# Kernel optimization log

Hardware: AMD Instinct MI355X
Metric: run time of the kernel (lower is better)

## Reference

```python
import jax, jax.numpy as jnp
import numpy as np
from jax import lax

CODEBOOK_DIM = 32
SCALE_SCHEDULE = [1, 2, 4, 8, 16, 32, 64, 128, 256, 512, 1024, 2048, 4096, 8192]
INV_TEMP = 100.0
COMMIT_W = 0.2
ENTROPY_W = 0.1
EPS_NORM = 1e-12
EPS_LOG = 1e-8


def setup_inputs() -> dict:
    key = jax.random.key(0)
    B, T, C = 32, 8192, CODEBOOK_DIM
    f_BTC = jax.random.normal(key, (B, T, C), dtype=jnp.float32)
    return {"f_BTC": f_BTC}


def _area_down(x, pt):
    # torch F.interpolate mode='area' on divisible sizes == average pooling
    B, T, C = x.shape
    if pt == T:
        return x
    return x.reshape(B, pt, T // pt, C).mean(axis=2)


def _linear_up(x, out_size):
    # torch F.interpolate mode='linear', align_corners=False
    B, in_size, C = x.shape
    if out_size == in_size:
        return x
    scale = in_size / out_size
    pos = (jnp.arange(out_size, dtype=jnp.float32) + 0.5) * scale - 0.5
    pos = jnp.clip(pos, 0.0, in_size - 1)
    lo = jnp.floor(pos).astype(jnp.int32)
    hi = jnp.minimum(lo + 1, in_size - 1)
    w = (pos - lo.astype(jnp.float32))[None, :, None]
    return x[:, lo] * (1.0 - w) + x[:, hi] * w


def _bsq_level(z):
    # normalize
    norm = jnp.sqrt(jnp.sum(z * z, axis=-1, keepdims=True))
    z = z / jnp.maximum(norm, EPS_NORM)
    q_scale = 1.0 / (CODEBOOK_DIM ** 0.5)
    zhat = jnp.where(z > 0, q_scale, -q_scale).astype(z.dtype)
    quant = z + lax.stop_gradient(zhat - z)  # STE
    # soft entropy loss
    p = jax.nn.sigmoid(-4.0 * z / (CODEBOOK_DIM ** 0.5) * INV_TEMP)
    ent = lambda c: -(c * jnp.log(c + EPS_LOG))
    per_sample = (ent(p) + ent(1.0 - p)).sum(axis=-1).mean()
    avg_p = p.mean(axis=(0, 1))  # [C]
    cb_ent = (ent(avg_p) + ent(1.0 - avg_p)).sum()
    entropy_penalty = (per_sample - cb_ent) / INV_TEMP
    commit = jnp.mean(((lax.stop_gradient(quant) - z) ** 2).sum(axis=-1))
    aux = entropy_penalty * ENTROPY_W + commit * COMMIT_W
    bits = (quant > 0).astype(jnp.int32)
    return quant, bits, aux


def reference(f_BTC):
    B, T, C = f_BTC.shape
    quantized_out = jnp.zeros_like(f_BTC)
    residual = f_BTC
    all_losses, all_bits = [], []
    for pt in SCALE_SCHEDULE:
        r = _area_down(residual, pt)
        quant, bits, loss = _bsq_level(r)
        q_up = _linear_up(quant, T)
        residual = residual - lax.stop_gradient(q_up)
        quantized_out = quantized_out + q_up
        all_bits.append(bits)
        all_losses.append(loss)
    return quantized_out, jnp.concatenate(all_bits, axis=1), jnp.stack(all_losses, axis=-1)
```

## Files before the change

kernel.cpp:

```cpp
#include <hip/hip_runtime.h>

#define B_DIM 32
#define T_DIM 8192
#define C_DIM 32
#define N_ELEM (B_DIM * T_DIM * C_DIM)
#define SUM_PT 16383
#define BITS_ELEM (B_DIM * SUM_PT * C_DIM)
#define NLEVEL 14
#define PARTW 2048
#define QSCALE 0.17677669529663687f
#define ALPHA  70.710678118654755f

#define OWN 128
#define HALO 16
#define MAXL (OWN + 2 * HALO)

__device__ __forceinline__ float entf(float x) { return -(x * __logf(x + 1e-8f)); }
__device__ __forceinline__ float qval(float bit) { return bit * (2.0f * QSCALE) - QSCALE; }

__device__ __forceinline__ float interp_pk(const unsigned int* __restrict__ pkbase,
                                           int ptj, float tpos, int c) {
    const float a = (float)ptj * (1.0f / (float)T_DIM);
    float pos = (tpos + 0.5f) * a - 0.5f;
    pos = fminf(fmaxf(pos, 0.0f), (float)(ptj - 1));
    const int lo = (int)pos;
    const int hi = min(lo + 1, ptj - 1);
    const float w = pos - (float)lo;
    const float b0 = (float)((pkbase[lo] >> c) & 1u);
    const float b1 = (float)((pkbase[hi] >> c) & 1u);
    return ((b0 * (1.0f - w) + b1 * w) * 2.0f - 1.0f) * QSCALE;
}

__device__ __forceinline__ float corr_mid_local(const unsigned int* __restrict__ bl,
                                                int ptk, int row, int c, int p0, int pN) {
    const float a = (float)ptk * (1.0f / (float)T_DIM);
    float pos = (float)(2 * row + 1) * a - 0.5f;
    pos = fminf(fmaxf(pos, 0.0f), (float)(ptk - 1));
    const int lo = (int)pos;
    const int hi = min(lo + 1, ptk - 1);
    const float w = pos - (float)lo;
    const int lol = min(max(lo - p0, 0), pN - 1);
    const int hil = min(max(hi - p0, 0), pN - 1);
    const float b0 = (float)((bl[lol] >> c) & 1u);
    const float b1 = (float)((bl[hil] >> c) & 1u);
    return ((b0 * (1.0f - w) + b1 * w) * 2.0f - 1.0f) * QSCALE;
}

__device__ float pooled_up_sum64(const float* base, int ptj, int m) {
    const int W = 64;
    const float a = (float)ptj * (1.0f / (float)T_DIM);
    const float p0 = ((float)(m * W) + 0.5f) * a - 0.5f;
    const float pmax = (float)(ptj - 1);
    float sum = 0.0f;
    int iL = 0;
    if (p0 < 0.0f) { iL = (int)ceilf(-p0 / a); if (iL > W) iL = W; }
    int iH = W - 1;
    if (p0 + (float)(W - 1) * a > pmax) {
        iH = (int)floorf((pmax - p0) / a);
        if (iH > W - 1) iH = W - 1;
        if (iH < -1) iH = -1;
    }
    if (iL > 0) sum += (float)iL * qval(base[0]);
    if (iH < W - 1) sum += (float)(W - 1 - iH) * qval(base[(size_t)(ptj - 1) * C_DIM]);
    if (iH >= iL) {
        const float pL = p0 + (float)iL * a;
        int l0 = (int)pL;
        if (l0 > ptj - 1) l0 = ptj - 1;
        const int is = (int)ceilf(((float)(l0 + 1) - p0) / a);
        const int endA = min(is - 1, iH);
        if (endA >= iL) {
            const int nA = endA - iL + 1;
            const float sI = 0.5f * (float)(iL + endA) * (float)nA;
            const float SA = (float)nA * (p0 - (float)l0) + a * sI;
            const float q0 = qval(base[(size_t)l0 * C_DIM]);
            const float q1 = qval(base[(size_t)min(l0 + 1, ptj - 1) * C_DIM]);
            sum += (float)nA * q0 + SA * (q1 - q0);
        }
        const int begB = max(is, iL);
        if (begB <= iH) {
            const int nB = iH - begB + 1;
            const float sI = 0.5f * (float)(begB + iH) * (float)nB;
            const float SB = (float)nB * (p0 - (float)(l0 + 1)) + a * sI;
            const float q1 = qval(base[(size_t)min(l0 + 1, ptj - 1) * C_DIM]);
            const float q2 = qval(base[(size_t)min(l0 + 2, ptj - 1) * C_DIM]);
            sum += (float)nB * q1 + SB * (q2 - q1);
        }
    }
    return sum;
}

template <int NT>
__device__ __forceinline__ void write_partials(float eAcc, float cAcc, float pAcc,
                                               float* partial, int level, int col) {
    __shared__ float sP[NT];
    __shared__ float sEC[NT / 16];
    __syncthreads();
    const int grp = threadIdx.x >> 5, c = threadIdx.x & 31;
    float eg = eAcc, cg = cAcc;
#pragma unroll
    for (int m = 16; m >= 1; m >>= 1) { eg += __shfl_xor(eg, m, 32); cg += __shfl_xor(cg, m, 32); }
    if (c == 0) { sEC[grp * 2] = eg; sEC[grp * 2 + 1] = cg; }
    sP[threadIdx.x] = pAcc;
    __syncthreads();
    float* base = partial + (size_t)level * 34 * PARTW;
    if (threadIdx.x < 32) {
        float ps = 0.f;
#pragma unroll
        for (int r = 0; r < NT / 32; ++r) ps += sP[threadIdx.x + r * 32];
        base[(size_t)(2 + threadIdx.x) * PARTW + col] = ps;
    }
    if (threadIdx.x == 0) {
        float se = 0.f, sc = 0.f;
#pragma unroll
        for (int g = 0; g < NT / 32; ++g) { se += sEC[2 * g]; sc += sEC[2 * g + 1]; }
        base[0 * PARTW + col] = se;
        base[(size_t)1 * PARTW + col] = sc;
    }
}

__device__ __forceinline__ float bsq_eval(float v, float& bit, float& pA, float& eA, float& cA) {
    float sq = v * v;
#pragma unroll
    for (int m = 16; m >= 1; m >>= 1) sq += __shfl_xor(sq, m, 32);
    const float z = v / fmaxf(sqrtf(sq), 1e-12f);
    bit = (z > 0.f) ? 1.0f : 0.0f;
    const float zh = (z > 0.f) ? QSCALE : -QSCALE;
    const float d = zh - z;
    cA += d * d;
    const float p = 1.0f / (1.0f + __expf(ALPHA * z));
    pA += p;
    eA += entf(p) + entf(1.0f - p);
    return zh;
}

__global__ void init_kernel(const float* __restrict__ f, float* __restrict__ F128) {
    const int b = blockIdx.x >> 7, m = blockIdx.x & 127;
    const int c = threadIdx.x & 31, grp = threadIdx.x >> 5;
    const float* fb = f + ((size_t)b * T_DIM + m * 64 + grp * 8) * C_DIM + c;
    float s = 0.f;
#pragma unroll
    for (int i = 0; i < 8; ++i) s += fb[i * C_DIM];
    __shared__ float red[8][32];
    red[grp][c] = s;
    __syncthreads();
    if (grp == 0) {
        float t = red[0][c] + red[1][c] + red[2][c] + red[3][c]
                + red[4][c] + red[5][c] + red[6][c] + red[7][c];
        F128[((size_t)b * 128 + m) * C_DIM + c] = t * (1.0f / 64.0f);
    }
}

__global__ __launch_bounds__(1024) void fused_small_kernel(const float* __restrict__ F128,
                                                           float* __restrict__ bits,
                                                           unsigned int* __restrict__ pkG,
                                                           float* __restrict__ partial) {
    const int b = blockIdx.x;
    __shared__ float P[128 * 32];
    __shared__ float qh[127 * 32];
    const int c = threadIdx.x & 31, grp = threadIdx.x >> 5;
    for (int i = threadIdx.x; i < 128 * 32; i += 1024) P[i] = F128[(size_t)b * 128 * 32 + i];
    __syncthreads();
    for (int k = 0; k < 8; ++k) {
        const int pt = 1 << k, W2 = 128 >> k;
        float pAcc = 0.f, eAcc = 0.f, cAcc = 0.f;
        for (int o = grp; o < pt; o += 32) {
            float v = 0.f;
            for (int i = 0; i < W2; ++i) v += P[(o * W2 + i) * 32 + c];
            v *= (1.0f / (float)W2);
            float bit;
            bsq_eval(v, bit, pAcc, eAcc, cAcc);
            bits[((size_t)b * SUM_PT + (pt - 1) + o) * C_DIM + c] = bit;
            const unsigned long long bal = __ballot(bit > 0.5f);
            if (c == 0)
                pkG[(size_t)b * 8192 + (pt - 1) + o] =
                    (threadIdx.x & 32) ? (unsigned)(bal >> 32) : (unsigned)bal;
            if (k < 7) qh[((pt - 1) + o) * 32 + c] = bit;
        }
        write_partials<1024>(eAcc, cAcc, pAcc, partial, k, b);
        if (k < 7) {
            __syncthreads();
            for (int m = grp; m < 128; m += 32)
                P[m * 32 + c] -= pooled_up_sum64(&qh[(pt - 1) * 32 + c], 1 << k, m) * (1.0f / 64.0f);
            __syncthreads();
        }
    }
}

__global__ __launch_bounds__(512) void chunk_kernel(const float* __restrict__ f,
                                                    float* __restrict__ bits,
                                                    unsigned int* __restrict__ pkG,
                                                    float* __restrict__ partial) {
    const int b = blockIdx.x >> 5;
    const int chunk = blockIdx.x & 31;
    const int r0 = chunk * OWN, r1 = r0 + OWN;
    const int L0 = max(0, r0 - HALO);
    const int L1 = min(4096, r1 + HALO);
    const int nL = L1 - L0;
    const int nSeg = nL >> 4;
    __shared__ float Rl[MAXL * 32];
    __shared__ unsigned int bitsL[310];
    __shared__ unsigned int pk07[255];
    __shared__ float segA[10][32], segB[10][32];
    const int c = threadIdx.x & 31, grp = threadIdx.x >> 5;

    const float* fb = f + ((size_t)b * T_DIM + (size_t)L0 * 2) * C_DIM;
    for (int i = threadIdx.x; i < nL * 8; i += 512) {
        const int row = i >> 3, c4 = i & 7;
        const float4 v0 = *(const float4*)(fb + (size_t)(2 * row) * 32 + c4 * 4);
        const float4 v1 = *(const float4*)(fb + (size_t)(2 * row + 1) * 32 + c4 * 4);
        float4 o;
        o.x = 0.5f * (v0.x + v1.x); o.y = 0.5f * (v0.y + v1.y);
        o.z = 0.5f * (v0.z + v1.z); o.w = 0.5f * (v0.w + v1.w);
        *(float4*)(Rl + row * 32 + c4 * 4) = o;
    }
    for (int i = threadIdx.x; i < 255; i += 512) pk07[i] = pkG[(size_t)b * 8192 + i];
    __syncthreads();

    for (int w = threadIdx.x; w < nSeg * 32; w += 512) {
        const int s = w >> 5, cc = w & 31;
        const int rg = L0 + s * 16;
        float c0 = 0.f, c1 = 0.f;
#pragma unroll
        for (int j = 0; j < 8; ++j) {
            const int ptj = 1 << j;
            c0 += interp_pk(pk07 + (ptj - 1), ptj, (float)(2 * rg) + 0.5f, cc);
            c1 += interp_pk(pk07 + (ptj - 1), ptj, (float)(2 * rg + 2) + 0.5f, cc);
        }
        segA[s][cc] = c0;
        segB[s][cc] = c1 - c0;
    }
    __syncthreads();
    for (int rl = grp; rl < nL; rl += 16) {
        const int s = rl >> 4;
        Rl[rl * 32 + c] -= fmaf((float)(rl & 15), segB[s][c], segA[s][c]);
    }
    __syncthreads();

    const int offs[5] = {0, 10, 30, 70, 150};
    for (int k = 8; k <= 12; ++k) {
        const int F = 4096 >> k;
        const int ptk = 1 << k;
        const int p0 = L0 / F, pN = nL / F;
        const int own0 = r0 / F, own1 = r1 / F;
        const int off = offs[k - 8];
        float pAcc = 0.f, eAcc = 0.f, cAcc = 0.f;
        for (int pl = grp; pl < pN; pl += 16) {
            float v = 0.f;
            for (int r = 0; r < F; ++r) v += Rl[(pl * F + r) * 32 + c];
            v *= (1.0f / (float)F);
            float sq = v * v;
#pragma unroll
            for (int m = 16; m >= 1; m >>= 1) sq += __shfl_xor(sq, m, 32);
            const float z = v / fmaxf(sqrtf(sq), 1e-12f);
            const unsigned long long bal = __ballot(z > 0.f);
            const unsigned int word = (threadIdx.x & 32) ? (unsigned)(bal >> 32) : (unsigned)bal;
            if (c == 0) bitsL[off + pl] = word;
            const int mg = p0 + pl;
            if (mg >= own0 && mg < own1) {
                bits[((size_t)b * SUM_PT + (ptk - 1) + mg) * C_DIM + c] = (z > 0.f) ? 1.f : 0.f;
                if (c == 0) pkG[(size_t)b * 8192 + (ptk - 1) + mg] = word;
                const float zh = (z > 0.f) ? QSCALE : -QSCALE;
                const float d = zh - z;
                cAcc += d * d;
                const float p = 1.0f / (1.0f + __expf(ALPHA * z));
                pAcc += p;
                eAcc += entf(p) + entf(1.0f - p);
            }
        }
        write_partials<512>(eAcc, cAcc, pAcc, partial, k, blockIdx.x);
        __syncthreads();
        if (k < 12) {
            for (int rl = grp; rl < nL; rl += 16)
                Rl[rl * 32 + c] -= corr_mid_local(bitsL + off, ptk, L0 + rl, c, p0, pN);
            __syncthreads();
        }
    }
}

__global__ __launch_bounds__(512) void final_kernel(const float* __restrict__ f,
                                                    float* __restrict__ outQ,
                                                    float* __restrict__ bits,
                                                    const unsigned int* __restrict__ pkG,
                                                    float* __restrict__ partial) {
    const int b = blockIdx.x >> 5;
    const int sub = blockIdx.x & 31;
    const int t0 = sub * 256;
    __shared__ unsigned int pkW[764];
    __shared__ float segA[16][32], segB[16][32];
    const int c = threadIdx.x & 31, grp = threadIdx.x >> 5;
    const unsigned int* pgb = pkG + (size_t)b * 8192;
    for (int i = threadIdx.x; i < 511; i += 512) pkW[i] = pgb[i];
    int woff[4], wbase[4];
    int o = 511;
#pragma unroll
    for (int j = 9; j <= 12; ++j) {
        const int ptj = 1 << j;
        const int w0 = max(0, ((t0 * ptj) >> 13) - 1);
        const int w1 = min(ptj - 1, (((t0 + 256) * ptj) >> 13) + 1);
        const int cnt = w1 - w0 + 1;
        for (int i = threadIdx.x; i < cnt; i += 512) pkW[o + i] = pgb[(ptj - 1) + w0 + i];
        woff[j - 9] = o;
        wbase[j - 9] = w0;
        o += cnt;
    }
    __syncthreads();
    for (int w = threadIdx.x; w < 512; w += 512) {
        const int s = w >> 5, cc = w & 31;
        const int tA = t0 + s * 16;
        float c0 = 0.f, c1 = 0.f;
#pragma unroll
        for (int j = 0; j <= 8; ++j) {
            const int ptj = 1 << j;
            c0 += interp_pk(pkW + (ptj - 1), ptj, (float)tA, cc);
            c1 += interp_pk(pkW + (ptj - 1), ptj, (float)(tA + 1), cc);
        }
        segA[s][cc] = c0;
        segB[s][cc] = c1 - c0;
    }
    __syncthreads();
    float pAcc = 0.f, eAcc = 0.f, cAcc = 0.f;
    for (int tt = grp; tt < 256; tt += 16) {
        const int t = t0 + tt;
        float up = fmaf((float)(tt & 15), segB[tt >> 4][c], segA[tt >> 4][c]);
#pragma unroll
        for (int j = 9; j <= 12; ++j) {
            const int ptj = 1 << j;
            const float a = (float)ptj * (1.0f / (float)T_DIM);
            float pos = ((float)t + 0.5f) * a - 0.5f;
            pos = fminf(fmaxf(pos, 0.0f), (float)(ptj - 1));
            const int lo = (int)pos;
            const int hi = min(lo + 1, ptj - 1);
            const float w = pos - (float)lo;
            const unsigned int* base = pkW + (woff[j - 9] - wbase[j - 9]);
            const float b0 = (float)((base[lo] >> c) & 1u);
            const float b1 = (float)((base[hi] >> c) & 1u);
            up += ((b0 * (1.0f - w) + b1 * w) * 2.0f - 1.0f) * QSCALE;
        }
        const size_t idx = ((size_t)b * T_DIM + t) * C_DIM + c;
        const float v = f[idx] - up;
        float bit;
        const float zh = bsq_eval(v, bit, pAcc, eAcc, cAcc);
        bits[((size_t)b * SUM_PT + (T_DIM - 1) + t) * C_DIM + c] = bit;
        outQ[idx] = up + zh;
    }
    write_partials<512>(eAcc, cAcc, pAcc, partial, 13, blockIdx.x);
}

__global__ void reduce_partials(const float* __restrict__ partial, float* __restrict__ acc) {
    const int level = blockIdx.x / 34;
    const int comp = blockIdx.x % 34;
    const int nblk = (level < 8) ? 32 : 1024;
    const float* s = partial + ((size_t)level * 34 + comp) * PARTW;
    float v = 0.f;
    for (int i = threadIdx.x; i < nblk; i += 64) v += s[i];
#pragma unroll
    for (int m = 32; m >= 1; m >>= 1) v += __shfl_xor(v, m, 64);
    if (threadIdx.x == 0) acc[level * 64 + comp] = v;
}

__global__ void finalize_kernel(const float* __restrict__ acc, float* __restrict__ outL) {
    const int k = threadIdx.x >> 5;
    const int c = threadIdx.x & 31;
    if (k >= NLEVEL) return;
    const float cnt = (float)(B_DIM << k);
    const float avg_p = acc[k * 64 + 2 + c] / cnt;
    float ec = entf(avg_p) + entf(1.0f - avg_p);
#pragma unroll
    for (int m = 16; m >= 1; m >>= 1) ec += __shfl_xor(ec, m, 32);
    if (c == 0) {
        const float per_sample = acc[k * 64 + 0] / cnt;
        const float commit = acc[k * 64 + 1] / cnt;
        const float pen = (per_sample - ec) * (1.0f / 100.0f);
        outL[k] = pen * 0.1f + commit * 0.2f;
    }
}

extern "C" void kernel_launch(void* const* d_in, const int* in_sizes, int n_in,
                              void* d_out, int out_size, void* d_ws, size_t ws_size,
                              hipStream_t stream) {
    (void)in_sizes; (void)n_in; (void)out_size; (void)ws_size;
    const float* f = (const float*)d_in[0];
    float* outQ = (float*)d_out;
    float* outBits = outQ + N_ELEM;
    float* outL = outBits + BITS_ELEM;

    float* partial = (float*)d_ws;
    float* acc = partial + (size_t)NLEVEL * 34 * PARTW;
    float* F128 = acc + NLEVEL * 64;
    unsigned int* pkG = (unsigned int*)(F128 + (size_t)B_DIM * 128 * C_DIM);

    init_kernel<<<B_DIM * 128, 256, 0, stream>>>(f, F128);
    fused_small_kernel<<<B_DIM, 1024, 0, stream>>>(F128, outBits, pkG, partial);
    chunk_kernel<<<B_DIM * 32, 512, 0, stream>>>(f, outBits, pkG, partial);
    final_kernel<<<B_DIM * 32, 512, 0, stream>>>(f, outQ, outBits, pkG, partial);
    reduce_partials<<<NLEVEL * 34, 64, 0, stream>>>(partial, acc);
    finalize_kernel<<<1, 512, 0, stream>>>(acc, outL);
}
```

Measured before the change: 171.1 us.

## Template per-level loops and fuse partial reduction with loss finalization

Turns the per-level loops in the small and chunk kernels into compile-time templated calls, so pooling widths and scale constants are constants and the inner pooling loops can be fully unrolled. The chunk kernel now reuses one bit buffer across levels and splits the residual-correction rows into contiguous ranges per group. The two tail kernels (partial reduction and loss finalization) are merged into a single one-block kernel to save a launch, but each thread now reduces up to 1024 values serially, which may lengthen the tail.

```diff
diff --git a/kernel.cpp b/kernel.cpp
--- a/kernel.cpp
+++ b/kernel.cpp
@@ -31,13 +31,14 @@
     return ((b0 * (1.0f - w) + b1 * w) * 2.0f - 1.0f) * QSCALE;
 }
 
+template <int PTK>
 __device__ __forceinline__ float corr_mid_local(const unsigned int* __restrict__ bl,
-                                                int ptk, int row, int c, int p0, int pN) {
-    const float a = (float)ptk * (1.0f / (float)T_DIM);
+                                                int row, int c, int p0, int pN) {
+    const float a = (float)PTK * (1.0f / (float)T_DIM);
     float pos = (float)(2 * row + 1) * a - 0.5f;
-    pos = fminf(fmaxf(pos, 0.0f), (float)(ptk - 1));
+    pos = fminf(fmaxf(pos, 0.0f), (float)(PTK - 1));
     const int lo = (int)pos;
-    const int hi = min(lo + 1, ptk - 1);
+    const int hi = min(lo + 1, PTK - 1);
     const float w = pos - (float)lo;
     const int lol = min(max(lo - p0, 0), pN - 1);
     const int hil = min(max(hi - p0, 0), pN - 1);
@@ -46,11 +47,12 @@
     return ((b0 * (1.0f - w) + b1 * w) * 2.0f - 1.0f) * QSCALE;
 }
 
-__device__ float pooled_up_sum64(const float* base, int ptj, int m) {
+template <int PTJ>
+__device__ float pooled_up_sum64(const float* base, int m) {
     const int W = 64;
-    const float a = (float)ptj * (1.0f / (float)T_DIM);
+    const float a = (float)PTJ * (1.0f / (float)T_DIM);
     const float p0 = ((float)(m * W) + 0.5f) * a - 0.5f;
-    const float pmax = (float)(ptj - 1);
+    const float pmax = (float)(PTJ - 1);
     float sum = 0.0f;
     int iL = 0;
     if (p0 < 0.0f) { iL = (int)ceilf(-p0 / a); if (iL > W) iL = W; }
@@ -61,11 +63,11 @@
         if (iH < -1) iH = -1;
     }
     if (iL > 0) sum += (float)iL * qval(base[0]);
-    if (iH < W - 1) sum += (float)(W - 1 - iH) * qval(base[(size_t)(ptj - 1) * C_DIM]);
+    if (iH < W - 1) sum += (float)(W - 1 - iH) * qval(base[(size_t)(PTJ - 1) * C_DIM]);
     if (iH >= iL) {
         const float pL = p0 + (float)iL * a;
         int l0 = (int)pL;
-        if (l0 > ptj - 1) l0 = ptj - 1;
+        if (l0 > PTJ - 1) l0 = PTJ - 1;
         const int is = (int)ceilf(((float)(l0 + 1) - p0) / a);
         const int endA = min(is - 1, iH);
         if (endA >= iL) {
@@ -73,7 +75,7 @@
             const float sI = 0.5f * (float)(iL + endA) * (float)nA;
             const float SA = (float)nA * (p0 - (float)l0) + a * sI;
             const float q0 = qval(base[(size_t)l0 * C_DIM]);
-            const float q1 = qval(base[(size_t)min(l0 + 1, ptj - 1) * C_DIM]);
+            const float q1 = qval(base[(size_t)min(l0 + 1, PTJ - 1) * C_DIM]);
             sum += (float)nA * q0 + SA * (q1 - q0);
         }
         const int begB = max(is, iL);
@@ -81,8 +83,8 @@
             const int nB = iH - begB + 1;
             const float sI = 0.5f * (float)(begB + iH) * (float)nB;
             const float SB = (float)nB * (p0 - (float)(l0 + 1)) + a * sI;
-            const float q1 = qval(base[(size_t)min(l0 + 1, ptj - 1) * C_DIM]);
-            const float q2 = qval(base[(size_t)min(l0 + 2, ptj - 1) * C_DIM]);
+            const float q1 = qval(base[(size_t)min(l0 + 1, PTJ - 1) * C_DIM]);
+            const float q2 = qval(base[(size_t)min(l0 + 2, PTJ - 1) * C_DIM]);
             sum += (float)nB * q1 + SB * (q2 - q1);
         }
     }
@@ -150,6 +152,36 @@
     }
 }
 
+template <int K>
+__device__ __forceinline__ void small_level(float* P, float* qh, float* __restrict__ bits,
+                                            unsigned int* __restrict__ pkG,
+                                            float* __restrict__ partial, int b,
+                                            int c, int grp) {
+    constexpr int pt = 1 << K, W2 = 128 >> K;
+    float pAcc = 0.f, eAcc = 0.f, cAcc = 0.f;
+    for (int o = grp; o < pt; o += 32) {
+        float v = 0.f;
+#pragma unroll
+        for (int i = 0; i < W2; ++i) v += P[(o * W2 + i) * 32 + c];
+        v *= (1.0f / (float)W2);
+        float bit;
+        bsq_eval(v, bit, pAcc, eAcc, cAcc);
+        bits[((size_t)b * SUM_PT + (pt - 1) + o) * C_DIM + c] = bit;
+        const unsigned long long bal = __ballot(bit > 0.5f);
+        if (c == 0)
+            pkG[(size_t)b * 8192 + (pt - 1) + o] =
+                (threadIdx.x & 32) ? (unsigned)(bal >> 32) : (unsigned)bal;
+        if (K < 7) qh[((pt - 1) + o) * 32 + c] = bit;
+    }
+    write_partials<1024>(eAcc, cAcc, pAcc, partial, K, b);
+    if (K < 7) {
+        __syncthreads();
+        for (int m = grp; m < 128; m += 32)
+            P[m * 32 + c] -= pooled_up_sum64<pt>(&qh[(pt - 1) * 32 + c], m) * (1.0f / 64.0f);
+        __syncthreads();
+    }
+}
+
 __global__ __launch_bounds__(1024) void fused_small_kernel(const float* __restrict__ F128,
                                                            float* __restrict__ bits,
                                                            unsigned int* __restrict__ pkG,
@@ -160,29 +192,60 @@
     const int c = threadIdx.x & 31, grp = threadIdx.x >> 5;
     for (int i = threadIdx.x; i < 128 * 32; i += 1024) P[i] = F128[(size_t)b * 128 * 32 + i];
     __syncthreads();
-    for (int k = 0; k < 8; ++k) {
-        const int pt = 1 << k, W2 = 128 >> k;
-        float pAcc = 0.f, eAcc = 0.f, cAcc = 0.f;
-        for (int o = grp; o < pt; o += 32) {
-            float v = 0.f;
-            for (int i = 0; i < W2; ++i) v += P[(o * W2 + i) * 32 + c];
-            v *= (1.0f / (float)W2);
-            float bit;
-            bsq_eval(v, bit, pAcc, eAcc, cAcc);
-            bits[((size_t)b * SUM_PT + (pt - 1) + o) * C_DIM + c] = bit;
-            const unsigned long long bal = __ballot(bit > 0.5f);
-            if (c == 0)
-                pkG[(size_t)b * 8192 + (pt - 1) + o] =
-                    (threadIdx.x & 32) ? (unsigned)(bal >> 32) : (unsigned)bal;
-            if (k < 7) qh[((pt - 1) + o) * 32 + c] = bit;
-        }
-        write_partials<1024>(eAcc, cAcc, pAcc, partial, k, b);
-        if (k < 7) {
-            __syncthreads();
-            for (int m = grp; m < 128; m += 32)
-                P[m * 32 + c] -= pooled_up_sum64(&qh[(pt - 1) * 32 + c], 1 << k, m) * (1.0f / 64.0f);
-            __syncthreads();
-        }
+    small_level<0>(P, qh, bits, pkG, partial, b, c, grp);
+    small_level<1>(P, qh, bits, pkG, partial, b, c, grp);
+    small_level<2>(P, qh, bits, pkG, partial, b, c, grp);
+    small_level<3>(P, qh, bits, pkG, partial, b, c, grp);
+    small_level<4>(P, qh, bits, pkG, partial, b, c, grp);
+    small_level<5>(P, qh, bits, pkG, partial, b, c, grp);
+    small_level<6>(P, qh, bits, pkG, partial, b, c, grp);
+    small_level<7>(P, qh, bits, pkG, partial, b, c, grp);
+}
+
+template <int K>
+__device__ __forceinline__ void chunk_level(float* Rl, unsigned int* bitsL,
+                                            float* __restrict__ bits,
+                                            unsigned int* __restrict__ pkG,
+                                            float* __restrict__ partial, int b,
+                                            int L0, int nL, int r0, int r1,
+                                            int c, int grp) {
+    constexpr int F = 4096 >> K;
+    constexpr int ptk = 1 << K;
+    const int p0 = L0 / F, pN = nL / F;
+    const int own0 = r0 / F, own1 = r1 / F;
+    float pAcc = 0.f, eAcc = 0.f, cAcc = 0.f;
+    for (int pl = grp; pl < pN; pl += 16) {
+        float v = 0.f;
+#pragma unroll
+        for (int r = 0; r < F; ++r) v += Rl[(pl * F + r) * 32 + c];
+        v *= (1.0f / (float)F);
+        float sq = v * v;
+#pragma unroll
+        for (int m = 16; m >= 1; m >>= 1) sq += __shfl_xor(sq, m, 32);
+        const float z = v / fmaxf(sqrtf(sq), 1e-12f);
+        const unsigned long long bal = __ballot(z > 0.f);
+        const unsigned int word = (threadIdx.x & 32) ? (unsigned)(bal >> 32) : (unsigned)bal;
+        if (c == 0) bitsL[pl] = word;
+        const int mg = p0 + pl;
+        if (mg >= own0 && mg < own1) {
+            bits[((size_t)b * SUM_PT + (ptk - 1) + mg) * C_DIM + c] = (z > 0.f) ? 1.f : 0.f;
+            if (c == 0) pkG[(size_t)b * 8192 + (ptk - 1) + mg] = word;
+            const float zh = (z > 0.f) ? QSCALE : -QSCALE;
+            const float d = zh - z;
+            cAcc += d * d;
+            const float p = 1.0f / (1.0f + __expf(ALPHA * z));
+            pAcc += p;
+            eAcc += entf(p) + entf(1.0f - p);
+        }
+    }
+    write_partials<512>(eAcc, cAcc, pAcc, partial, K, blockIdx.x);
+    if (K < 12) {
+        const int rowsPer = (nL + 15) >> 4;
+        const int rA = grp * rowsPer;
+        const int rB = min(rA + rowsPer, nL);
+        for (int rl = rA; rl < rB; ++rl)
+            Rl[rl * 32 + c] -= corr_mid_local<ptk>(bitsL, L0 + rl, c, p0, pN);
+        __syncthreads();
     }
 }
 
@@ -198,7 +261,7 @@
     const int nL = L1 - L0;
     const int nSeg = nL >> 4;
     __shared__ float Rl[MAXL * 32];
-    __shared__ unsigned int bitsL[310];
+    __shared__ unsigned int bitsL[MAXL];
     __shared__ unsigned int pk07[255];
     __shared__ float segA[10][32], segB[10][32];
     const int c = threadIdx.x & 31, grp = threadIdx.x >> 5;
@@ -236,45 +299,11 @@
     }
     __syncthreads();
 
-    const int offs[5] = {0, 10, 30, 70, 150};
-    for (int k = 8; k <= 12; ++k) {
-        const int F = 4096 >> k;
-        const int ptk = 1 << k;
-        const int p0 = L0 / F, pN = nL / F;
-        const int own0 = r0 / F, own1 = r1 / F;
-        const int off = offs[k - 8];
-        float pAcc = 0.f, eAcc = 0.f, cAcc = 0.f;
-        for (int pl = grp; pl < pN; pl += 16) {
-            float v = 0.f;
-            for (int r = 0; r < F; ++r) v += Rl[(pl * F + r) * 32 + c];
-            v *= (1.0f / (float)F);
-            float sq = v * v;
-#pragma unroll
-            for (int m = 16; m >= 1; m >>= 1) sq += __shfl_xor(sq, m, 32);
-            const float z = v / fmaxf(sqrtf(sq), 1e-12f);
-            const unsigned long long bal = __ballot(z > 0.f);
-            const unsigned int word = (threadIdx.x & 32) ? (unsigned)(bal >> 32) : (unsigned)bal;
-            if (c == 0) bitsL[off + pl] = word;
-            const int mg = p0 + pl;
-            if (mg >= own0 && mg < own1) {
-                bits[((size_t)b * SUM_PT + (ptk - 1) + mg) * C_DIM + c] = (z > 0.f) ? 1.f : 0.f;
-                if (c == 0) pkG[(size_t)b * 8192 + (ptk - 1) + mg] = word;
-                const float zh = (z > 0.f) ? QSCALE : -QSCALE;
-                const float d = zh - z;
-                cAcc += d * d;
-                const float p = 1.0f / (1.0f + __expf(ALPHA * z));
-                pAcc += p;
-                eAcc += entf(p) + entf(1.0f - p);
-            }
-        }
-        write_partials<512>(eAcc, cAcc, pAcc, partial, k, blockIdx.x);
-        __syncthreads();
-        if (k < 12) {
-            for (int rl = grp; rl < nL; rl += 16)
-                Rl[rl * 32 + c] -= corr_mid_local(bitsL + off, ptk, L0 + rl, c, p0, pN);
-            __syncthreads();
-        }
-    }
+    chunk_level<8>(Rl, bitsL, bits, pkG, partial, b, L0, nL, r0, r1, c, grp);
+    chunk_level<9>(Rl, bitsL, bits, pkG, partial, b, L0, nL, r0, r1, c, grp);
+    chunk_level<10>(Rl, bitsL, bits, pkG, partial, b, L0, nL, r0, r1, c, grp);
+    chunk_level<11>(Rl, bitsL, bits, pkG, partial, b, L0, nL, r0, r1, c, grp);
+    chunk_level<12>(Rl, bitsL, bits, pkG, partial, b, L0, nL, r0, r1, c, grp);
 }
 
 __global__ __launch_bounds__(512) void final_kernel(const float* __restrict__ f,
@@ -346,32 +375,34 @@
     write_partials<512>(eAcc, cAcc, pAcc, partial, 13, blockIdx.x);
 }
 
-__global__ void reduce_partials(const float* __restrict__ partial, float* __restrict__ acc) {
-    const int level = blockIdx.x / 34;
-    const int comp = blockIdx.x % 34;
-    const int nblk = (level < 8) ? 32 : 1024;
-    const float* s = partial + ((size_t)level * 34 + comp) * PARTW;
-    float v = 0.f;
-    for (int i = threadIdx.x; i < nblk; i += 64) v += s[i];
-#pragma unroll
-    for (int m = 32; m >= 1; m >>= 1) v += __shfl_xor(v, m, 64);
-    if (threadIdx.x == 0) acc[level * 64 + comp] = v;
-}
-
-__global__ void finalize_kernel(const float* __restrict__ acc, float* __restrict__ outL) {
-    const int k = threadIdx.x >> 5;
-    const int c = threadIdx.x & 31;
-    if (k >= NLEVEL) return;
-    const float cnt = (float)(B_DIM << k);
-    const float avg_p = acc[k * 64 + 2 + c] / cnt;
-    float ec = entf(avg_p) + entf(1.0f - avg_p);
-#pragma unroll
-    for (int m = 16; m >= 1; m >>= 1) ec += __shfl_xor(ec, m, 32);
-    if (c == 0) {
-        const float per_sample = acc[k * 64 + 0] / cnt;
-        const float commit = acc[k * 64 + 1] / cnt;
-        const float pen = (per_sample - ec) * (1.0f / 100.0f);
-        outL[k] = pen * 0.1f + commit * 0.2f;
+__global__ __launch_bounds__(1024) void reduce_finalize(const float* __restrict__ partial,
+                                                        float* __restrict__ outL) {
+    __shared__ float accS[NLEVEL * 34];
+    const int tid = threadIdx.x;
+    if (tid < NLEVEL * 34) {
+        const int level = tid / 34, comp = tid % 34;
+        const int nblk = (level < 8) ? 32 : 1024;
+        const float* s = partial + ((size_t)level * 34 + comp) * PARTW;
+        float v0 = 0.f, v1 = 0.f, v2 = 0.f, v3 = 0.f;
+        for (int i = 0; i < nblk; i += 4) {
+            v0 += s[i]; v1 += s[i + 1]; v2 += s[i + 2]; v3 += s[i + 3];
+        }
+        accS[tid] = (v0 + v1) + (v2 + v3);
+    }
+    __syncthreads();
+    const int k = tid >> 5, c = tid & 31;
+    if (k < NLEVEL) {
+        const float cnt = (float)(B_DIM << k);
+        const float avg_p = accS[k * 34 + 2 + c] / cnt;
+        float ec = entf(avg_p) + entf(1.0f - avg_p);
+#pragma unroll
+        for (int m = 16; m >= 1; m >>= 1) ec += __shfl_xor(ec, m, 32);
+        if (c == 0) {
+            const float per_sample = accS[k * 34 + 0] / cnt;
+            const float commit = accS[k * 34 + 1] / cnt;
+            const float pen = (per_sample - ec) * (1.0f / 100.0f);
+            outL[k] = pen * 0.1f + commit * 0.2f;
+        }
     }
 }
 
@@ -393,6 +424,5 @@
     fused_small_kernel<<<B_DIM, 1024, 0, stream>>>(F128, outBits, pkG, partial);
     chunk_kernel<<<B_DIM * 32, 512, 0, stream>>>(f, outBits, pkG, partial);
     final_kernel<<<B_DIM * 32, 512, 0, stream>>>(f, outQ, outBits, pkG, partial);
-    reduce_partials<<<NLEVEL * 34, 64, 0, stream>>>(partial, acc);
-    finalize_kernel<<<1, 512, 0, stream>>>(acc, outL);
-}
+    reduce_finalize<<<1, 1024, 0, stream>>>(partial, outL);
+}
```

Result: slower. 184.7 us (+7.9%).

## Precompute interpolation tables, template chunk levels, merge reduce and finalize

Applied to the files above, without the earlier changes.

Adds shared-memory tables of interpolation weights and packed lo/hi indices to chunk_kernel and final_kernel. Each per-element upsample correction then reads these tables instead of recomputing clamps and floors. The chunk level loop becomes a templated function so the pooling loop has a compile-time trip count and can be unrolled. The two tail kernels are fused into one single-block reduce_finalize launch, which drops a launch at the cost of serial per-thread summation. The chunk path also drops the barrier between writing bitsL and the correction that reads it, which may introduce a race unless write_partials synchronises internally.

```diff
diff --git a/kernel.cpp b/kernel.cpp
--- a/kernel.cpp
+++ b/kernel.cpp
@@ -28,21 +28,6 @@
     const float w = pos - (float)lo;
     const float b0 = (float)((pkbase[lo] >> c) & 1u);
     const float b1 = (float)((pkbase[hi] >> c) & 1u);
-    return ((b0 * (1.0f - w) + b1 * w) * 2.0f - 1.0f) * QSCALE;
-}
-
-__device__ __forceinline__ float corr_mid_local(const unsigned int* __restrict__ bl,
-                                                int ptk, int row, int c, int p0, int pN) {
-    const float a = (float)ptk * (1.0f / (float)T_DIM);
-    float pos = (float)(2 * row + 1) * a - 0.5f;
-    pos = fminf(fmaxf(pos, 0.0f), (float)(ptk - 1));
-    const int lo = (int)pos;
-    const int hi = min(lo + 1, ptk - 1);
-    const float w = pos - (float)lo;
-    const int lol = min(max(lo - p0, 0), pN - 1);
-    const int hil = min(max(hi - p0, 0), pN - 1);
-    const float b0 = (float)((bl[lol] >> c) & 1u);
-    const float b1 = (float)((bl[hil] >> c) & 1u);
     return ((b0 * (1.0f - w) + b1 * w) * 2.0f - 1.0f) * QSCALE;
 }
 
@@ -186,6 +171,56 @@
     }
 }
 
+template <int K>
+__device__ __forceinline__ void chunk_level(float* Rl, unsigned int* bitsL,
+                                            const float* wT, const int* iT,
+                                            float* __restrict__ bits,
+                                            unsigned int* __restrict__ pkG,
+                                            float* __restrict__ partial, int b,
+                                            int L0, int nL, int r0, int r1,
+                                            int c, int grp) {
+    constexpr int F = 4096 >> K;
+    constexpr int ptk = 1 << K;
+    const int p0 = L0 / F, pN = nL / F;
+    const int own0 = r0 / F, own1 = r1 / F;
+    float pAcc = 0.f, eAcc = 0.f, cAcc = 0.f;
+    for (int pl = grp; pl < pN; pl += 16) {
+        float v = 0.f;
+#pragma unroll
+        for (int r = 0; r < F; ++r) v += Rl[(pl * F + r) * 32 + c];
+        v *= (1.0f / (float)F);
+        float sq = v * v;
+#pragma unroll
+        for (int m = 16; m >= 1; m >>= 1) sq += __shfl_xor(sq, m, 32);
+        const float z = v / fmaxf(sqrtf(sq), 1e-12f);
+        const unsigned long long bal = __ballot(z > 0.f);
+        const unsigned int word = (threadIdx.x & 32) ? (unsigned)(bal >> 32) : (unsigned)bal;
+        if (c == 0) bitsL[pl] = word;
+        const int mg = p0 + pl;
+        if (mg >= own0 && mg < own1) {
+            bits[((size_t)b * SUM_PT + (ptk - 1) + mg) * C_DIM + c] = (z > 0.f) ? 1.f : 0.f;
+            if (c == 0) pkG[(size_t)b * 8192 + (ptk - 1) + mg] = word;
+            const float zh = (z > 0.f) ? QSCALE : -QSCALE;
+            const float d = zh - z;
+            cAcc += d * d;
+            const float p = 1.0f / (1.0f + __expf(ALPHA * z));
+            pAcc += p;
+            eAcc += entf(p) + entf(1.0f - p);
+        }
+    }
+    write_partials<512>(eAcc, cAcc, pAcc, partial, K, blockIdx.x);
+    if (K < 12) {
+        for (int rl = grp; rl < nL; rl += 16) {
+            const float w = wT[rl];
+            const int pk = iT[rl];
+            const float b0 = (float)((bitsL[pk & 0xFFFF] >> c) & 1u);
+            const float b1 = (float)((bitsL[pk >> 16] >> c) & 1u);
+            Rl[rl * 32 + c] -= ((b0 * (1.0f - w) + b1 * w) * 2.0f - 1.0f) * QSCALE;
+        }
+        __syncthreads();
+    }
+}
+
 __global__ __launch_bounds__(512) void chunk_kernel(const float* __restrict__ f,
                                                     float* __restrict__ bits,
                                                     unsigned int* __restrict__ pkG,
@@ -198,9 +233,11 @@
     const int nL = L1 - L0;
     const int nSeg = nL >> 4;
     __shared__ float Rl[MAXL * 32];
-    __shared__ unsigned int bitsL[310];
+    __shared__ unsigned int bitsL[MAXL];
     __shared__ unsigned int pk07[255];
     __shared__ float segA[10][32], segB[10][32];
+    __shared__ float wT[4 * MAXL];
+    __shared__ int iT[4 * MAXL];
     const int c = threadIdx.x & 31, grp = threadIdx.x >> 5;
 
     const float* fb = f + ((size_t)b * T_DIM + (size_t)L0 * 2) * C_DIM;
@@ -214,6 +251,21 @@
         *(float4*)(Rl + row * 32 + c4 * 4) = o;
     }
     for (int i = threadIdx.x; i < 255; i += 512) pk07[i] = pkG[(size_t)b * 8192 + i];
+    for (int idx = threadIdx.x; idx < 4 * nL; idx += 512) {
+        const int lvl = idx / nL, rl = idx - lvl * nL;
+        const int ptk = 256 << lvl;
+        const int F = 4096 / ptk;
+        const int p0 = L0 / F, pN = nL / F;
+        const float a = (float)ptk * (1.0f / (float)T_DIM);
+        float pos = (float)(2 * (L0 + rl) + 1) * a - 0.5f;
+        pos = fminf(fmaxf(pos, 0.0f), (float)(ptk - 1));
+        const int lo = (int)pos;
+        const int hi = min(lo + 1, ptk - 1);
+        wT[idx] = pos - (float)lo;
+        const int lol = min(max(lo - p0, 0), pN - 1);
+        const int hil = min(max(hi - p0, 0), pN - 1);
+        iT[idx] = lol | (hil << 16);
+    }
     __syncthreads();
 
     for (int w = threadIdx.x; w < nSeg * 32; w += 512) {
@@ -236,45 +288,11 @@
     }
     __syncthreads();
 
-    const int offs[5] = {0, 10, 30, 70, 150};
-    for (int k = 8; k <= 12; ++k) {
-        const int F = 4096 >> k;
-        const int ptk = 1 << k;
-        const int p0 = L0 / F, pN = nL / F;
-        const int own0 = r0 / F, own1 = r1 / F;
-        const int off = offs[k - 8];
-        float pAcc = 0.f, eAcc = 0.f, cAcc = 0.f;
-        for (int pl = grp; pl < pN; pl += 16) {
-            float v = 0.f;
-            for (int r = 0; r < F; ++r) v += Rl[(pl * F + r) * 32 + c];
-            v *= (1.0f / (float)F);
-            float sq = v * v;
-#pragma unroll
-            for (int m = 16; m >= 1; m >>= 1) sq += __shfl_xor(sq, m, 32);
-            const float z = v / fmaxf(sqrtf(sq), 1e-12f);
-            const unsigned long long bal = __ballot(z > 0.f);
-            const unsigned int word = (threadIdx.x & 32) ? (unsigned)(bal >> 32) : (unsigned)bal;
-            if (c == 0) bitsL[off + pl] = word;
-            const int mg = p0 + pl;
-            if (mg >= own0 && mg < own1) {
-                bits[((size_t)b * SUM_PT + (ptk - 1) + mg) * C_DIM + c] = (z > 0.f) ? 1.f : 0.f;
-                if (c == 0) pkG[(size_t)b * 8192 + (ptk - 1) + mg] = word;
-                const float zh = (z > 0.f) ? QSCALE : -QSCALE;
-                const float d = zh - z;
-                cAcc += d * d;
-                const float p = 1.0f / (1.0f + __expf(ALPHA * z));
-                pAcc += p;
-                eAcc += entf(p) + entf(1.0f - p);
-            }
-        }
-        write_partials<512>(eAcc, cAcc, pAcc, partial, k, blockIdx.x);
-        __syncthreads();
-        if (k < 12) {
-            for (int rl = grp; rl < nL; rl += 16)
-                Rl[rl * 32 + c] -= corr_mid_local(bitsL + off, ptk, L0 + rl, c, p0, pN);
-            __syncthreads();
-        }
-    }
+    chunk_level<8>(Rl, bitsL, wT + 0 * nL, iT + 0 * nL, bits, pkG, partial, b, L0, nL, r0, r1, c, grp);
+    chunk_level<9>(Rl, bitsL, wT + 1 * nL, iT + 1 * nL, bits, pkG, partial, b, L0, nL, r0, r1, c, grp);
+    chunk_level<10>(Rl, bitsL, wT + 2 * nL, iT + 2 * nL, bits, pkG, partial, b, L0, nL, r0, r1, c, grp);
+    chunk_level<11>(Rl, bitsL, wT + 3 * nL, iT + 3 * nL, bits, pkG, partial, b, L0, nL, r0, r1, c, grp);
+    chunk_level<12>(Rl, bitsL, wT, iT, bits, pkG, partial, b, L0, nL, r0, r1, c, grp);
 }
 
 __global__ __launch_bounds__(512) void final_kernel(const float* __restrict__ f,
@@ -287,6 +305,8 @@
     const int t0 = sub * 256;
     __shared__ unsigned int pkW[764];
     __shared__ float segA[16][32], segB[16][32];
+    __shared__ float wT2[4 * 256];
+    __shared__ int iT2[4 * 256];
     const int c = threadIdx.x & 31, grp = threadIdx.x >> 5;
     const unsigned int* pgb = pkG + (size_t)b * 8192;
     for (int i = threadIdx.x; i < 511; i += 512) pkW[i] = pgb[i];
@@ -303,6 +323,18 @@
         wbase[j - 9] = w0;
         o += cnt;
     }
+    for (int idx = threadIdx.x; idx < 4 * 256; idx += 512) {
+        const int lvl = idx >> 8, tt = idx & 255;
+        const int ptj = 1 << (9 + lvl);
+        const float a = (float)ptj * (1.0f / (float)T_DIM);
+        float pos = ((float)(t0 + tt) + 0.5f) * a - 0.5f;
+        pos = fminf(fmaxf(pos, 0.0f), (float)(ptj - 1));
+        const int lo = (int)pos;
+        const int hi = min(lo + 1, ptj - 1);
+        wT2[idx] = pos - (float)lo;
+        const int base = woff[lvl] - wbase[lvl];
+        iT2[idx] = (base + lo) | ((base + hi) << 16);
+    }
     __syncthreads();
     for (int w = threadIdx.x; w < 512; w += 512) {
         const int s = w >> 5, cc = w & 31;
@@ -323,17 +355,11 @@
         const int t = t0 + tt;
         float up = fmaf((float)(tt & 15), segB[tt >> 4][c], segA[tt >> 4][c]);
 #pragma unroll
-        for (int j = 9; j <= 12; ++j) {
-            const int ptj = 1 << j;
-            const float a = (float)ptj * (1.0f / (float)T_DIM);
-            float pos = ((float)t + 0.5f) * a - 0.5f;
-            pos = fminf(fmaxf(pos, 0.0f), (float)(ptj - 1));
-            const int lo = (int)pos;
-            const int hi = min(lo + 1, ptj - 1);
-            const float w = pos - (float)lo;
-            const unsigned int* base = pkW + (woff[j - 9] - wbase[j - 9]);
-            const float b0 = (float)((base[lo] >> c) & 1u);
-            const float b1 = (float)((base[hi] >> c) & 1u);
+        for (int lvl = 0; lvl < 4; ++lvl) {
+            const float w = wT2[lvl * 256 + tt];
+            const int pk = iT2[lvl * 256 + tt];
+            const float b0 = (float)((pkW[pk & 0xFFFF] >> c) & 1u);
+            const float b1 = (float)((pkW[pk >> 16] >> c) & 1u);
             up += ((b0 * (1.0f - w) + b1 * w) * 2.0f - 1.0f) * QSCALE;
         }
         const size_t idx = ((size_t)b * T_DIM + t) * C_DIM + c;
@@ -346,32 +372,34 @@
     write_partials<512>(eAcc, cAcc, pAcc, partial, 13, blockIdx.x);
 }
 
-__global__ void reduce_partials(const float* __restrict__ partial, float* __restrict__ acc) {
-    const int level = blockIdx.x / 34;
-    const int comp = blockIdx.x % 34;
-    const int nblk = (level < 8) ? 32 : 1024;
-    const float* s = partial + ((size_t)level * 34 + comp) * PARTW;
-    float v = 0.f;
-    for (int i = threadIdx.x; i < nblk; i += 64) v += s[i];
-#pragma unroll
-    for (int m = 32; m >= 1; m >>= 1) v += __shfl_xor(v, m, 64);
-    if (threadIdx.x == 0) acc[level * 64 + comp] = v;
-}
-
-__global__ void finalize_kernel(const float* __restrict__ acc, float* __restrict__ outL) {
-    const int k = threadIdx.x >> 5;
-    const int c = threadIdx.x & 31;
-    if (k >= NLEVEL) return;
-    const float cnt = (float)(B_DIM << k);
-    const float avg_p = acc[k * 64 + 2 + c] / cnt;
-    float ec = entf(avg_p) + entf(1.0f - avg_p);
-#pragma unroll
-    for (int m = 16; m >= 1; m >>= 1) ec += __shfl_xor(ec, m, 32);
-    if (c == 0) {
-        const float per_sample = acc[k * 64 + 0] / cnt;
-        const float commit = acc[k * 64 + 1] / cnt;
-        const float pen = (per_sample - ec) * (1.0f / 100.0f);
-        outL[k] = pen * 0.1f + commit * 0.2f;
+__global__ __launch_bounds__(1024) void reduce_finalize(const float* __restrict__ partial,
+                                                        float* __restrict__ outL) {
+    __shared__ float accS[NLEVEL * 34];
+    const int tid = threadIdx.x;
+    if (tid < NLEVEL * 34) {
+        const int level = tid / 34, comp = tid % 34;
+        const int nblk = (level < 8) ? 32 : 1024;
+        const float* s = partial + ((size_t)level * 34 + comp) * PARTW;
+        float v0 = 0.f, v1 = 0.f, v2 = 0.f, v3 = 0.f;
+        for (int i = 0; i < nblk; i += 4) {
+            v0 += s[i]; v1 += s[i + 1]; v2 += s[i + 2]; v3 += s[i + 3];
+        }
+        accS[tid] = (v0 + v1) + (v2 + v3);
+    }
+    __syncthreads();
+    const int k = tid >> 5, c = tid & 31;
+    if (k < NLEVEL) {
+        const float cnt = (float)(B_DIM << k);
+        const float avg_p = accS[k * 34 + 2 + c] / cnt;
+        float ec = entf(avg_p) + entf(1.0f - avg_p);
+#pragma unroll
+        for (int m = 16; m >= 1; m >>= 1) ec += __shfl_xor(ec, m, 32);
+        if (c == 0) {
+            const float per_sample = accS[k * 34 + 0] / cnt;
+            const float commit = accS[k * 34 + 1] / cnt;
+            const float pen = (per_sample - ec) * (1.0f / 100.0f);
+            outL[k] = pen * 0.1f + commit * 0.2f;
+        }
     }
 }
 
@@ -393,6 +421,5 @@
     fused_small_kernel<<<B_DIM, 1024, 0, stream>>>(F128, outBits, pkG, partial);
     chunk_kernel<<<B_DIM * 32, 512, 0, stream>>>(f, outBits, pkG, partial);
     final_kernel<<<B_DIM * 32, 512, 0, stream>>>(f, outQ, outBits, pkG, partial);
-    reduce_partials<<<NLEVEL * 34, 64, 0, stream>>>(partial, acc);
-    finalize_kernel<<<1, 512, 0, stream>>>(acc, outL);
-}
+    reduce_finalize<<<1, 1024, 0, stream>>>(partial, outL);
+}
```

After: 184.1 us. 1.08x slower.
